# Kernel tuning notes

Measured on AMD Instinct MI355X. Metric: run time of the kernel, lower is better.

## Reference

```python
import jax, jax.numpy as jnp
import numpy as np

EPS = 1e-6

def _ln(x, g, b):
    mu = jnp.mean(x, axis=-1, keepdims=True)
    var = jnp.mean(jnp.square(x - mu), axis=-1, keepdims=True)
    return (x - mu) * jax.lax.rsqrt(var + EPS) * g + b

def setup_inputs() -> dict:
    key = jax.random.key(0)
    ks = jax.random.split(key, 8)
    B, T, D = 4, 4096, 1024
    H = 16
    Dff = 4 * D
    s = 1.0 / np.sqrt(D)
    sf = 1.0 / np.sqrt(Dff)
    return {
        "x": jax.random.normal(ks[0], (B, T, D), dtype=jnp.float32),
        "wq": jax.random.uniform(ks[1], (D, D), jnp.float32, -s, s),
        "wk": jax.random.uniform(ks[2], (D, D), jnp.float32, -s, s),
        "wv": jax.random.uniform(ks[3], (D, D), jnp.float32, -s, s),
        "wo": jax.random.uniform(ks[4], (D, D), jnp.float32, -s, s),
        "ln1_g": jnp.ones((D,), jnp.float32),
        "ln1_b": jnp.zeros((D,), jnp.float32),
        "w1": jax.random.uniform(ks[5], (D, Dff), jnp.float32, -s, s),
        "b1": jnp.zeros((Dff,), jnp.float32),
        "w2": jax.random.uniform(ks[6], (Dff, D), jnp.float32, -sf, sf),
        "b2": jnp.zeros((D,), jnp.float32),
        "ln2_g": jnp.ones((D,), jnp.float32),
        "ln2_b": jnp.zeros((D,), jnp.float32),
    }

def reference(x, wq, wk, wv, wo, ln1_g, ln1_b, w1, b1, w2, b2, ln2_g, ln2_b):
    B, T, D = x.shape
    H = 16
    dk = D // H
    x1 = _ln(x, ln1_g, ln1_b)
    q = (x1 @ wq).reshape(B, T, H, dk)
    k = (x1 @ wk).reshape(B, T, H, dk)
    v = (x1 @ wv).reshape(B, T, H, dk)
    # NOTE: faithful to source -- attention mixes HEADS at each token position
    # attn[b,t,h,g] = softmax_g( sum_d q[b,t,h,d]*k[b,t,g,d] / sqrt(dk) )
    attn = jax.nn.softmax(jnp.einsum('bthd,btgd->bthg', q / np.sqrt(dk), k), axis=-1)
    o = jnp.einsum('bthg,btgd->bthd', attn, v)
    # faithful head-major reshape: transpose(1,2).contiguous().view(B,T,-1)
    o = jnp.transpose(o, (0, 2, 1, 3)).reshape(B, T, H * dk)
    o = o @ wo
    q2 = _ln(o + x, ln1_g, ln1_b)  # same layer_norm params reused
    h = jax.nn.gelu(q2 @ w1 + b1, approximate=False)
    y = h @ w2 + b2 + q2
    return _ln(y, ln2_g, ln2_b)
```

## Files before the change

kernel.cpp:

```cpp
#include <hip/hip_runtime.h>


typedef __attribute__((ext_vector_type(8))) short s16x8;
typedef __attribute__((ext_vector_type(4))) short s16x4;
typedef __attribute__((ext_vector_type(16))) float f32x16;

__device__ __forceinline__ short f2bf(float x) {
  unsigned u = __builtin_bit_cast(unsigned, x);
  u = (u + 0x7FFFu + ((u >> 16) & 1u)) >> 16;
  return (short)u;
}
__device__ __forceinline__ float bf2f(short s) {
  unsigned u = ((unsigned)(unsigned short)s) << 16;
  return __builtin_bit_cast(float, u);
}

__device__ __forceinline__ void ld_g2l16(const short* g, short* l) {
  __builtin_amdgcn_global_load_lds(
      (const __attribute__((address_space(1))) void*)g,
      (__attribute__((address_space(3))) void*)l, 16, 0, 0);
}

__device__ __forceinline__ float fast_gelu(float v) {
  float y = 0.7978845608f * (v + 0.044715f * v * v * v);
  float ay = fabsf(y);
  float t = __expf(-2.0f * ay);
  float th = (1.0f - t) * __frcp_rn(1.0f + t);
  th = (y >= 0.f) ? th : -th;
  return 0.5f * v * (1.0f + th);
}

template <int EPI>
__global__ __launch_bounds__(256, 4) void gemm_bt(
    const short* __restrict__ A, const short* __restrict__ BT,
    void* __restrict__ outp, const float* __restrict__ bias, int M, int N,
    int K) {
  __shared__ __align__(16) short As[2][128 * 32];
  __shared__ __align__(16) short Bs[2][128 * 32];

  const int lane = threadIdx.x & 63;
  const int wave = threadIdx.x >> 6;
  const int bm = blockIdx.x, bn = blockIdx.y;
  const int m31 = lane & 31;
  const int h = lane >> 5;
  const int wm = (wave >> 1) * 64;
  const int wn = (wave & 1) * 64;

  f32x16 acc[2][2];
#pragma unroll
  for (int i = 0; i < 2; i++)
#pragma unroll
    for (int j = 0; j < 2; j++)
#pragma unroll
      for (int r = 0; r < 16; r++) acc[i][j][r] = 0.f;

  const int srow = lane >> 2;
  const int sch = (lane & 3) ^ ((lane >> 4) & 3);
  const short* gA = A + (size_t)(bm * 128) * K + sch * 8;
  const short* gB = BT + (size_t)(bn * 128) * K + sch * 8;

  const int xkey = (m31 >> 2) & 3;

  const int iters = K >> 5;

#pragma unroll
  for (int c = 0; c < 2; c++) {
    const int s = wave * 2 + c;
    ld_g2l16(gA + (size_t)(s * 16 + srow) * K, As[0] + s * 512);
    ld_g2l16(gB + (size_t)(s * 16 + srow) * K, Bs[0] + s * 512);
  }

  for (int n = 0; n < iters; n++) {
    __syncthreads();

    if (n + 1 < iters) {
      const int kk = (n + 1) << 5;
      const int nb2 = (n + 1) & 1;
#pragma unroll
      for (int c = 0; c < 2; c++) {
        const int s = wave * 2 + c;
        ld_g2l16(gA + (size_t)(s * 16 + srow) * K + kk, As[nb2] + s * 512);
        ld_g2l16(gB + (size_t)(s * 16 + srow) * K + kk, Bs[nb2] + s * 512);
      }
    }

    const int cb = n & 1;
#pragma unroll
    for (int ks = 0; ks < 2; ks++) {
      const int g = ks * 2 + h;
      const int co = (g ^ xkey) * 8;
      s16x8 a8[2], b8[2];
#pragma unroll
      for (int i = 0; i < 2; i++)
        a8[i] = *(const s16x8*)(As[cb] + (wm + i * 32 + m31) * 32 + co);
#pragma unroll
      for (int j = 0; j < 2; j++)
        b8[j] = *(const s16x8*)(Bs[cb] + (wn + j * 32 + m31) * 32 + co);
#pragma unroll
      for (int i = 0; i < 2; i++)
#pragma unroll
        for (int j = 0; j < 2; j++)
          acc[i][j] = __builtin_amdgcn_mfma_f32_32x32x16_bf16(
              a8[i], b8[j], acc[i][j], 0, 0, 0);
    }
  }

  const int mb = bm * 128 + wm, nb = bn * 128 + wn;
#pragma unroll
  for (int i = 0; i < 2; i++) {
#pragma unroll
    for (int j = 0; j < 2; j++) {
#pragma unroll
      for (int r = 0; r < 16; r++) {
        const size_t row =
            (size_t)(mb + i * 32 + (r & 3) + 8 * (r >> 2) + 4 * h);
        const int col = nb + j * 32 + m31;
        float v = acc[i][j][r];
        if constexpr (EPI == 0) {
          ((short*)outp)[row * N + col] = f2bf(v);
        } else if constexpr (EPI == 1) {
          ((float*)outp)[row * N + col] = v;
        } else if constexpr (EPI == 2) {
          v += bias[col];
          ((short*)outp)[row * N + col] = f2bf(fast_gelu(v));
        } else {
          float prev = ((float*)outp)[row * N + col];
          v += prev;
          if (bias) v += bias[col];
          ((float*)outp)[row * N + col] = v;
        }
      }
    }
  }
}

__global__ __launch_bounds__(256) void ln_k(
    const float* __restrict__ in, const float* __restrict__ add,
    const float* __restrict__ g, const float* __restrict__ b,
    float* __restrict__ outf, short* __restrict__ outb) {
  const int row = blockIdx.x;
  const size_t off = (size_t)row * 1024;
  const int t = threadIdx.x;
  float4 v = ((const float4*)(in + off))[t];
  if (add) {
    float4 w = ((const float4*)(add + off))[t];
    v.x += w.x; v.y += w.y; v.z += w.z; v.w += w.w;
  }
  float s = v.x + v.y + v.z + v.w;
  float ss = v.x * v.x + v.y * v.y + v.z * v.z + v.w * v.w;
#pragma unroll
  for (int o = 32; o > 0; o >>= 1) {
    s += __shfl_xor(s, o, 64);
    ss += __shfl_xor(ss, o, 64);
  }
  __shared__ float ps[4], pss[4];
  const int lane = t & 63, wave = t >> 6;
  if (lane == 0) { ps[wave] = s; pss[wave] = ss; }
  __syncthreads();
  s = ps[0] + ps[1] + ps[2] + ps[3];
  ss = pss[0] + pss[1] + pss[2] + pss[3];
  const float mean = s * (1.0f / 1024.0f);
  const float var = ss * (1.0f / 1024.0f) - mean * mean;
  const float rstd = rsqrtf(var + 1e-6f);
  const float4 gv = ((const float4*)g)[t];
  const float4 bv = ((const float4*)b)[t];
  float4 o4;
  o4.x = (v.x - mean) * rstd * gv.x + bv.x;
  o4.y = (v.y - mean) * rstd * gv.y + bv.y;
  o4.z = (v.z - mean) * rstd * gv.z + bv.z;
  o4.w = (v.w - mean) * rstd * gv.w + bv.w;
  if (outf) ((float4*)(outf + off))[t] = o4;
  if (outb) {
    s16x4 ob;
    ob[0] = f2bf(o4.x); ob[1] = f2bf(o4.y);
    ob[2] = f2bf(o4.z); ob[3] = f2bf(o4.w);
    *(s16x4*)(outb + off + t * 4) = ob;
  }
}

__global__ __launch_bounds__(256) void wconv_t(const float* __restrict__ W,
                                               short* __restrict__ WT, int K,
                                               int N) {
  __shared__ float tile[32][33];
  const int t = threadIdx.x;
  const int c = t & 31, r = t >> 5;
  const int n0 = blockIdx.x * 32, k0 = blockIdx.y * 32;
#pragma unroll
  for (int rr = r; rr < 32; rr += 8)
    tile[rr][c] = W[(size_t)(k0 + rr) * N + n0 + c];
  __syncthreads();
#pragma unroll
  for (int rr = r; rr < 32; rr += 8)
    WT[(size_t)(n0 + rr) * K + k0 + c] = f2bf(tile[c][rr]);
}

__global__ __launch_bounds__(256) void attn_k(const short* __restrict__ qkv,
                                              short* __restrict__ omix) {
  __shared__ float Qs[4][16][64];
  __shared__ float Ks[4][16][64];
  __shared__ float Vs[4][16][64];
  __shared__ float Ps[4][16][16];
  const int lane = threadIdx.x & 63;
  const int wave = threadIdx.x >> 6;
  const int tok = blockIdx.x * 4 + wave;
  const short* base = qkv + (size_t)tok * 3072;

#pragma unroll
  for (int half = 0; half < 2; half++) {
    const int e = half * 512 + lane * 8;
    const int h = e >> 6, d = e & 63;
    s16x8 rq = *(const s16x8*)(base + e);
    s16x8 rk = *(const s16x8*)(base + 1024 + e);
    s16x8 rv = *(const s16x8*)(base + 2048 + e);
#pragma unroll
    for (int j = 0; j < 8; j++) {
      Qs[wave][h][d + j] = bf2f(rq[j]);
      Ks[wave][h][d + j] = bf2f(rk[j]);
      Vs[wave][h][d + j] = bf2f(rv[j]);
    }
  }
  __syncthreads();

  const int h = lane & 15;
  const int g0 = (lane >> 4) * 4;
  float sc[4] = {0.f, 0.f, 0.f, 0.f};
  for (int d = 0; d < 64; d++) {
    const float qv = Qs[wave][h][d];
#pragma unroll
    for (int i = 0; i < 4; i++) sc[i] += qv * Ks[wave][g0 + i][d];
  }
#pragma unroll
  for (int i = 0; i < 4; i++) sc[i] *= 0.125f;
  float m = fmaxf(fmaxf(sc[0], sc[1]), fmaxf(sc[2], sc[3]));
  m = fmaxf(m, __shfl_xor(m, 16, 64));
  m = fmaxf(m, __shfl_xor(m, 32, 64));
  float e[4], sum = 0.f;
#pragma unroll
  for (int i = 0; i < 4; i++) { e[i] = __expf(sc[i] - m); sum += e[i]; }
  sum += __shfl_xor(sum, 16, 64);
  sum += __shfl_xor(sum, 32, 64);
  const float inv = __frcp_rn(sum);
#pragma unroll
  for (int i = 0; i < 4; i++) Ps[wave][h][g0 + i] = e[i] * inv;
  __syncthreads();

  const int d0 = (lane >> 4) * 16;
  float o[16];
#pragma unroll
  for (int dd = 0; dd < 16; dd++) o[dd] = 0.f;
  for (int gg = 0; gg < 16; gg++) {
    const float pv = Ps[wave][h][gg];
#pragma unroll
    for (int dd = 0; dd < 16; dd++) o[dd] += pv * Vs[wave][gg][d0 + dd];
  }

  const int b = tok >> 12, t = tok & 4095;
  const size_t dst =
      ((size_t)(b * 4096 + h * 256 + (t >> 4))) * 1024 + (t & 15) * 64 + d0;
  s16x8 w0, w1;
#pragma unroll
  for (int j = 0; j < 8; j++) { w0[j] = f2bf(o[j]); w1[j] = f2bf(o[8 + j]); }
  *(s16x8*)(omix + dst) = w0;
  *(s16x8*)(omix + dst + 8) = w1;
}

extern "C" void kernel_launch(void* const* d_in, const int* in_sizes, int n_in,
                              void* d_out, int out_size, void* d_ws,
                              size_t ws_size, hipStream_t stream) {
  const float* x    = (const float*)d_in[0];
  const float* wq   = (const float*)d_in[1];
  const float* wk   = (const float*)d_in[2];
  const float* wv   = (const float*)d_in[3];
  const float* wo   = (const float*)d_in[4];
  const float* ln1g = (const float*)d_in[5];
  const float* ln1b = (const float*)d_in[6];
  const float* w1   = (const float*)d_in[7];
  const float* b1   = (const float*)d_in[8];
  const float* w2   = (const float*)d_in[9];
  const float* b2   = (const float*)d_in[10];
  const float* ln2g = (const float*)d_in[11];
  const float* ln2b = (const float*)d_in[12];
  float* out = (float*)d_out;

  char* ws = (char*)d_ws;
  const size_t MB = 1024ull * 1024ull;
  const size_t NEEDED = 152 * MB;
  if (ws_size < NEEDED) return;

  short* QKV  = (short*)(ws + 0);
  short* Q2B  = (short*)(ws + 0);
  short* Hbuf = (short*)(ws + 32 * MB);
  short* X1 = (short*)(ws + 96 * MB);
  short* WQKVT = (short*)(ws + 128 * MB);
  short* WOT   = (short*)(ws + 134 * MB);
  short* W1T   = (short*)(ws + 136 * MB);
  short* W2aT  = (short*)(ws + 144 * MB);
  short* W2bT  = (short*)(ws + 148 * MB);

  const dim3 B256(256);

  wconv_t<<<dim3(32, 32), B256, 0, stream>>>(wq, WQKVT, 1024, 1024);
  wconv_t<<<dim3(32, 32), B256, 0, stream>>>(wk, WQKVT + 1024 * 1024, 1024, 1024);
  wconv_t<<<dim3(32, 32), B256, 0, stream>>>(wv, WQKVT + 2048 * 1024, 1024, 1024);
  wconv_t<<<dim3(32, 32), B256, 0, stream>>>(wo, WOT, 1024, 1024);
  wconv_t<<<dim3(128, 32), B256, 0, stream>>>(w1, W1T, 1024, 4096);
  wconv_t<<<dim3(32, 64), B256, 0, stream>>>(w2, W2aT, 2048, 1024);
  wconv_t<<<dim3(32, 64), B256, 0, stream>>>(w2 + 2048 * 1024, W2bT, 2048, 1024);

  ln_k<<<16384, B256, 0, stream>>>(x, nullptr, ln1g, ln1b, nullptr, X1);

  gemm_bt<0><<<dim3(128, 24), B256, 0, stream>>>(X1, WQKVT, QKV, nullptr,
                                                 16384, 3072, 1024);

  attn_k<<<4096, B256, 0, stream>>>(QKV, X1);

  gemm_bt<1><<<dim3(128, 8), B256, 0, stream>>>(X1, WOT, out, nullptr, 16384,
                                                1024, 1024);

  ln_k<<<16384, B256, 0, stream>>>(out, x, ln1g, ln1b, out, Q2B);

  gemm_bt<2><<<dim3(128, 16), B256, 0, stream>>>(Q2B, W1T, Hbuf, b1, 16384,
                                                 2048, 1024);
  gemm_bt<4><<<dim3(128, 8), B256, 0, stream>>>(Hbuf, W2aT, out, nullptr,
                                                16384, 1024, 2048);

  gemm_bt<2><<<dim3(128, 16), B256, 0, stream>>>(Q2B, W1T + 2048 * 1024, Hbuf,
                                                 b1 + 2048, 16384, 2048, 1024);
  gemm_bt<4><<<dim3(128, 8), B256, 0, stream>>>(Hbuf, W2bT, out, b2, 16384,
                                                1024, 2048);

  ln_k<<<16384, B256, 0, stream>>>(out, nullptr, ln2g, ln2b, out, nullptr);
}
```

Before: 901.5 us.

## Replace 128x128 GEMM with 256x256-tile ping-pong pipelined MFMA16 kernel

Replaces the 128x128-tile, 256-thread bf16 GEMM with a 256x256-tile, 512-thread kernel. It uses 16x16x32 MFMAs, a K step of 64, double-buffered 128KB dynamic LDS, and staged global-to-LDS loads interleaved across four compute phases with barriers and s_setprio. It also adds an XCD-aware block-index remap so that tiles are grouped per chiplet. The goal is more data reuse per tile and overlap of loads with compute, at the cost of lower occupancy and a hardcoded bm = wg & 63, which assumes M = 16384.

After: 833.9 us. 7.5% less time.

```diff
diff --git a/kernel.cpp b/kernel.cpp
--- a/kernel.cpp
+++ b/kernel.cpp
@@ -3,7 +3,7 @@
 
 typedef __attribute__((ext_vector_type(8))) short s16x8;
 typedef __attribute__((ext_vector_type(4))) short s16x4;
-typedef __attribute__((ext_vector_type(16))) float f32x16;
+typedef __attribute__((ext_vector_type(4))) float f32x4;
 
 __device__ __forceinline__ short f2bf(float x) {
   unsigned u = __builtin_bit_cast(unsigned, x);
@@ -30,92 +30,172 @@
   return 0.5f * v * (1.0f + th);
 }
 
+#define MFMA16(va, vb, vc) \
+  __builtin_amdgcn_mfma_f32_16x16x32_bf16(va, vb, vc, 0, 0, 0)
+
 template <int EPI>
-__global__ __launch_bounds__(256, 4) void gemm_bt(
+__global__ __launch_bounds__(512, 2) void gemm256(
     const short* __restrict__ A, const short* __restrict__ BT,
-    void* __restrict__ outp, const float* __restrict__ bias, int M, int N,
-    int K) {
-  __shared__ __align__(16) short As[2][128 * 32];
-  __shared__ __align__(16) short Bs[2][128 * 32];
-
-  const int lane = threadIdx.x & 63;
-  const int wave = threadIdx.x >> 6;
-  const int bm = blockIdx.x, bn = blockIdx.y;
-  const int m31 = lane & 31;
-  const int h = lane >> 5;
-  const int wm = (wave >> 1) * 64;
-  const int wn = (wave & 1) * 64;
-
-  f32x16 acc[2][2];
-#pragma unroll
-  for (int i = 0; i < 2; i++)
-#pragma unroll
-    for (int j = 0; j < 2; j++)
-#pragma unroll
-      for (int r = 0; r < 16; r++) acc[i][j][r] = 0.f;
-
-  const int srow = lane >> 2;
-  const int sch = (lane & 3) ^ ((lane >> 4) & 3);
-  const short* gA = A + (size_t)(bm * 128) * K + sch * 8;
-  const short* gB = BT + (size_t)(bn * 128) * K + sch * 8;
-
-  const int xkey = (m31 >> 2) & 3;
-
-  const int iters = K >> 5;
-
-#pragma unroll
-  for (int c = 0; c < 2; c++) {
-    const int s = wave * 2 + c;
-    ld_g2l16(gA + (size_t)(s * 16 + srow) * K, As[0] + s * 512);
-    ld_g2l16(gB + (size_t)(s * 16 + srow) * K, Bs[0] + s * 512);
-  }
-
-  for (int n = 0; n < iters; n++) {
-    __syncthreads();
-
-    if (n + 1 < iters) {
-      const int kk = (n + 1) << 5;
-      const int nb2 = (n + 1) & 1;
-#pragma unroll
-      for (int c = 0; c < 2; c++) {
-        const int s = wave * 2 + c;
-        ld_g2l16(gA + (size_t)(s * 16 + srow) * K + kk, As[nb2] + s * 512);
-        ld_g2l16(gB + (size_t)(s * 16 + srow) * K + kk, Bs[nb2] + s * 512);
+    void* __restrict__ outp, const float* __restrict__ bias, int N, int K) {
+  extern __shared__ __align__(16) short smem[];
+
+  const int t = threadIdx.x;
+  const int lane = t & 63, w = t >> 6;
+  const int wm = w >> 2, wn = w & 3;
+
+  const int nwg = gridDim.x, q8 = nwg >> 3;
+  const int wg = ((int)blockIdx.x & 7) * q8 + ((int)blockIdx.x >> 3);
+  const int bm = wg & 63;
+  const int bn = wg >> 6;
+
+  short* Ac = smem;
+  short* An = smem + 16384;
+  short* Bc = smem + 32768;
+  short* Bn = smem + 49152;
+
+  const int l8 = lane >> 3;
+  const int lcw = ((lane & 7) ^ l8) * 8;
+  const short* gA = A + (size_t)(bm * 256 + w * 8 + l8) * K + lcw;
+  const short* gB = BT + (size_t)(bn * 256 + w * 8 + l8) * K + lcw;
+  const int lb = w * 512;
+
+  auto stage = [&](const short* g, short* buf, int h, int kt) {
+    const size_t go = (size_t)(h * 128) * K + (size_t)kt * 64;
+    ld_g2l16(g + go, buf + h * 8192 + lb);
+    ld_g2l16(g + go + (size_t)64 * K, buf + h * 8192 + 4096 + lb);
+  };
+
+  const int fr = lane & 15, fc = lane >> 4;
+  const int baseA = (wm * 128 + fr) * 64;
+  const int baseB = (wn * 64 + fr) * 64;
+  const int sl0 = (fc ^ (fr & 7)) * 8;
+  const int sl1 = ((4 + fc) ^ (fr & 7)) * 8;
+
+  f32x4 acc[8][4];
+#pragma unroll
+  for (int m = 0; m < 8; ++m)
+#pragma unroll
+    for (int n = 0; n < 4; ++n) acc[m][n] = (f32x4){0.f, 0.f, 0.f, 0.f};
+
+  s16x8 a[4][2], b0[2][2], b1[2][2];
+
+  const int nt = K >> 6;
+
+  stage(gA, Ac, 0, 0);
+  stage(gA, Ac, 1, 0);
+  stage(gB, Bc, 0, 0);
+  stage(gB, Bc, 1, 0);
+  if (nt > 1) {
+    stage(gA, An, 0, 1);
+    stage(gB, Bn, 0, 1);
+    asm volatile("s_waitcnt vmcnt(4)" ::: "memory");
+  } else {
+    asm volatile("s_waitcnt vmcnt(0)" ::: "memory");
+  }
+  __builtin_amdgcn_s_barrier();
+  asm volatile("" ::: "memory");
+
+  for (int u = 0; u < nt; ++u) {
+#pragma unroll
+    for (int mi = 0; mi < 4; ++mi) {
+      a[mi][0] = *(const s16x8*)(Ac + baseA + mi * 1024 + sl0);
+      a[mi][1] = *(const s16x8*)(Ac + baseA + mi * 1024 + sl1);
+    }
+#pragma unroll
+    for (int ni = 0; ni < 2; ++ni) {
+      b0[ni][0] = *(const s16x8*)(Bc + baseB + ni * 1024 + sl0);
+      b0[ni][1] = *(const s16x8*)(Bc + baseB + ni * 1024 + sl1);
+    }
+    if (u + 1 < nt) stage(gA, An, 1, u + 1);
+    __builtin_amdgcn_s_barrier();
+    asm volatile("s_waitcnt lgkmcnt(0)" ::: "memory");
+    __builtin_amdgcn_s_setprio(1);
+#pragma unroll
+    for (int mi = 0; mi < 4; ++mi)
+#pragma unroll
+      for (int ni = 0; ni < 2; ++ni) {
+        acc[mi][ni] = MFMA16(a[mi][0], b0[ni][0], acc[mi][ni]);
+        acc[mi][ni] = MFMA16(a[mi][1], b0[ni][1], acc[mi][ni]);
       }
-    }
-
-    const int cb = n & 1;
-#pragma unroll
-    for (int ks = 0; ks < 2; ks++) {
-      const int g = ks * 2 + h;
-      const int co = (g ^ xkey) * 8;
-      s16x8 a8[2], b8[2];
-#pragma unroll
-      for (int i = 0; i < 2; i++)
-        a8[i] = *(const s16x8*)(As[cb] + (wm + i * 32 + m31) * 32 + co);
-#pragma unroll
-      for (int j = 0; j < 2; j++)
-        b8[j] = *(const s16x8*)(Bs[cb] + (wn + j * 32 + m31) * 32 + co);
-#pragma unroll
-      for (int i = 0; i < 2; i++)
-#pragma unroll
-        for (int j = 0; j < 2; j++)
-          acc[i][j] = __builtin_amdgcn_mfma_f32_32x32x16_bf16(
-              a8[i], b8[j], acc[i][j], 0, 0, 0);
-    }
-  }
-
-  const int mb = bm * 128 + wm, nb = bn * 128 + wn;
-#pragma unroll
-  for (int i = 0; i < 2; i++) {
-#pragma unroll
-    for (int j = 0; j < 2; j++) {
-#pragma unroll
-      for (int r = 0; r < 16; r++) {
-        const size_t row =
-            (size_t)(mb + i * 32 + (r & 3) + 8 * (r >> 2) + 4 * h);
-        const int col = nb + j * 32 + m31;
-        float v = acc[i][j][r];
+    __builtin_amdgcn_s_setprio(0);
+    __builtin_amdgcn_s_barrier();
+    asm volatile("" ::: "memory");
+
+#pragma unroll
+    for (int ni = 0; ni < 2; ++ni) {
+      b1[ni][0] = *(const s16x8*)(Bc + baseB + 2048 + ni * 1024 + sl0);
+      b1[ni][1] = *(const s16x8*)(Bc + baseB + 2048 + ni * 1024 + sl1);
+    }
+    if (u + 1 < nt) stage(gB, Bn, 1, u + 1);
+    __builtin_amdgcn_s_barrier();
+    asm volatile("s_waitcnt lgkmcnt(0)" ::: "memory");
+    __builtin_amdgcn_s_setprio(1);
+#pragma unroll
+    for (int mi = 0; mi < 4; ++mi)
+#pragma unroll
+      for (int ni = 0; ni < 2; ++ni) {
+        acc[mi][2 + ni] = MFMA16(a[mi][0], b1[ni][0], acc[mi][2 + ni]);
+        acc[mi][2 + ni] = MFMA16(a[mi][1], b1[ni][1], acc[mi][2 + ni]);
+      }
+    __builtin_amdgcn_s_setprio(0);
+    __builtin_amdgcn_s_barrier();
+    asm volatile("" ::: "memory");
+
+#pragma unroll
+    for (int mi = 0; mi < 4; ++mi) {
+      a[mi][0] = *(const s16x8*)(Ac + baseA + 4096 + mi * 1024 + sl0);
+      a[mi][1] = *(const s16x8*)(Ac + baseA + 4096 + mi * 1024 + sl1);
+    }
+    if (u + 2 < nt) stage(gB, Bc, 0, u + 2);
+    __builtin_amdgcn_s_barrier();
+    asm volatile("s_waitcnt lgkmcnt(0)" ::: "memory");
+    __builtin_amdgcn_s_setprio(1);
+#pragma unroll
+    for (int mi = 0; mi < 4; ++mi)
+#pragma unroll
+      for (int ni = 0; ni < 2; ++ni) {
+        acc[4 + mi][2 + ni] = MFMA16(a[mi][0], b1[ni][0], acc[4 + mi][2 + ni]);
+        acc[4 + mi][2 + ni] = MFMA16(a[mi][1], b1[ni][1], acc[4 + mi][2 + ni]);
+      }
+    __builtin_amdgcn_s_setprio(0);
+    __builtin_amdgcn_s_barrier();
+    asm volatile("" ::: "memory");
+
+    if (u + 2 < nt) stage(gA, Ac, 0, u + 2);
+    __builtin_amdgcn_s_setprio(1);
+#pragma unroll
+    for (int mi = 0; mi < 4; ++mi)
+#pragma unroll
+      for (int ni = 0; ni < 2; ++ni) {
+        acc[4 + mi][ni] = MFMA16(a[mi][0], b0[ni][0], acc[4 + mi][ni]);
+        acc[4 + mi][ni] = MFMA16(a[mi][1], b0[ni][1], acc[4 + mi][ni]);
+      }
+    __builtin_amdgcn_s_setprio(0);
+    if (u + 2 < nt) {
+      asm volatile("s_waitcnt vmcnt(4)" ::: "memory");
+    } else {
+      asm volatile("s_waitcnt vmcnt(0)" ::: "memory");
+    }
+    __builtin_amdgcn_s_barrier();
+    asm volatile("" ::: "memory");
+
+    short* tp = Ac; Ac = An; An = tp;
+    tp = Bc; Bc = Bn; Bn = tp;
+  }
+
+  const int mb = bm * 256 + wm * 128;
+  const int nb = bn * 256 + wn * 64;
+  const int cr = (lane >> 4) * 4;
+  const int cc = lane & 15;
+#pragma unroll
+  for (int m = 0; m < 8; ++m) {
+#pragma unroll
+    for (int n = 0; n < 4; ++n) {
+#pragma unroll
+      for (int r = 0; r < 4; ++r) {
+        const size_t row = (size_t)(mb + m * 16 + cr + r);
+        const size_t col = (size_t)(nb + n * 16 + cc);
+        float v = acc[m][n][r];
         if constexpr (EPI == 0) {
           ((short*)outp)[row * N + col] = f2bf(v);
         } else if constexpr (EPI == 1) {
@@ -298,6 +378,29 @@
   short* W2bT  = (short*)(ws + 148 * MB);
 
   const dim3 B256(256);
+  const dim3 B512(512);
+  const unsigned LDS = 131072;
+
+  static bool attr_done = false;
+  if (!attr_done) {
+    attr_done = true;
+    void (*k0)(const short*, const short*, void*, const float*, int, int) =
+        gemm256<0>;
+    void (*k1)(const short*, const short*, void*, const float*, int, int) =
+        gemm256<1>;
+    void (*k2)(const short*, const short*, void*, const float*, int, int) =
+        gemm256<2>;
+    void (*k4)(const short*, const short*, void*, const float*, int, int) =
+        gemm256<4>;
+    (void)hipFuncSetAttribute((const void*)k0,
+        hipFuncAttributeMaxDynamicSharedMemorySize, (int)LDS);
+    (void)hipFuncSetAttribute((const void*)k1,
+        hipFuncAttributeMaxDynamicSharedMemorySize, (int)LDS);
+    (void)hipFuncSetAttribute((const void*)k2,
+        hipFuncAttributeMaxDynamicSharedMemorySize, (int)LDS);
+    (void)hipFuncSetAttribute((const void*)k4,
+        hipFuncAttributeMaxDynamicSharedMemorySize, (int)LDS);
+  }
 
   wconv_t<<<dim3(32, 32), B256, 0, stream>>>(wq, WQKVT, 1024, 1024);
   wconv_t<<<dim3(32, 32), B256, 0, stream>>>(wk, WQKVT + 1024 * 1024, 1024, 1024);
@@ -309,25 +412,25 @@
 
   ln_k<<<16384, B256, 0, stream>>>(x, nullptr, ln1g, ln1b, nullptr, X1);
 
-  gemm_bt<0><<<dim3(128, 24), B256, 0, stream>>>(X1, WQKVT, QKV, nullptr,
-                                                 16384, 3072, 1024);
+  gemm256<0><<<dim3(768), B512, LDS, stream>>>(X1, WQKVT, QKV, nullptr,
+                                               3072, 1024);
 
   attn_k<<<4096, B256, 0, stream>>>(QKV, X1);
 
-  gemm_bt<1><<<dim3(128, 8), B256, 0, stream>>>(X1, WOT, out, nullptr, 16384,
-                                                1024, 1024);
+  gemm256<1><<<dim3(256), B512, LDS, stream>>>(X1, WOT, out, nullptr,
+                                               1024, 1024);
 
   ln_k<<<16384, B256, 0, stream>>>(out, x, ln1g, ln1b, out, Q2B);
 
-  gemm_bt<2><<<dim3(128, 16), B256, 0, stream>>>(Q2B, W1T, Hbuf, b1, 16384,
-                                                 2048, 1024);
-  gemm_bt<4><<<dim3(128, 8), B256, 0, stream>>>(Hbuf, W2aT, out, nullptr,
-                                                16384, 1024, 2048);
-
-  gemm_bt<2><<<dim3(128, 16), B256, 0, stream>>>(Q2B, W1T + 2048 * 1024, Hbuf,
-                                                 b1 + 2048, 16384, 2048, 1024);
-  gemm_bt<4><<<dim3(128, 8), B256, 0, stream>>>(Hbuf, W2bT, out, b2, 16384,
-                                                1024, 2048);
+  gemm256<2><<<dim3(512), B512, LDS, stream>>>(Q2B, W1T, Hbuf, b1,
+                                               2048, 1024);
+  gemm256<4><<<dim3(256), B512, LDS, stream>>>(Hbuf, W2aT, out, nullptr,
+                                               1024, 2048);
+
+  gemm256<2><<<dim3(512), B512, LDS, stream>>>(Q2B, W1T + 2048 * 1024, Hbuf,
+                                               b1 + 2048, 2048, 1024);
+  gemm256<4><<<dim3(256), B512, LDS, stream>>>(Hbuf, W2bT, out, b2,
+                                               1024, 2048);
 
   ln_k<<<16384, B256, 0, stream>>>(out, nullptr, ln2g, ln2b, out, nullptr);
 }
```
